# Kernel tuning notes

Measured on AMD Instinct MI355X. Metric: run time of the kernel, lower is better.

Reference implementation:

```python
import jax, jax.numpy as jnp
import numpy as np

B, S, D = 2, 2048, 1024
H = 16
HD = D // H  # 64
SCALE = HD ** -0.5


def setup_inputs() -> dict:
    key = jax.random.key(0)
    ks = jax.random.split(key, 9)
    init = lambda k, shape: jax.random.normal(k, shape, dtype=jnp.float32) * (1.0 / np.sqrt(shape[-1]))
    return {
        "x": jax.random.normal(ks[0], (B, S, D), dtype=jnp.float32),
        "wq": init(ks[1], (D, D)), "bq": jnp.zeros((D,), jnp.float32),
        "wk": init(ks[2], (D, D)), "bk": jnp.zeros((D,), jnp.float32),
        "wv": init(ks[3], (D, D)), "bv": jnp.zeros((D,), jnp.float32),
        "wo": init(ks[4], (D, D)), "bo": jnp.zeros((D,), jnp.float32),
    }


def reference(x, wq, bq, wk, bk, wv, bv, wo, bo):
    b, s, d = x.shape
    # projections -> [b, h, s, hd]
    q = (x @ wq + bq).reshape(b, s, H, HD).transpose(0, 2, 1, 3)
    k = (x @ wk + bk).reshape(b, s, H, HD).transpose(0, 2, 1, 3)
    v = (x @ wv + bv).reshape(b, s, H, HD).transpose(0, 2, 1, 3)
    # full causal attention (chunked loop in original computes exactly this)
    scores = jnp.einsum("bhqd,bhkd->bhqk", q, k) * SCALE
    causal = jnp.tril(jnp.ones((s, s), dtype=bool))
    scores = jnp.where(causal, scores, -jnp.inf)
    weights = jax.nn.softmax(scores, axis=-1)
    out = jnp.einsum("bhqk,bhkd->bhqd", weights, v)
    out = out.transpose(0, 2, 1, 3).reshape(b, s, d)
    return out @ wo + bo
```

## Files before the change

kernel.cpp:

```cpp
#include <hip/hip_runtime.h>
#include <hip/hip_bf16.h>
#include <cstdint>

#define B_  2
#define S_  2048
#define D_  1024
#define H_  16
#define HD_ 64
#define M_  (B_ * S_)
static constexpr float SC_LOG2E = 0.125f * 1.44269504088896f;

typedef __bf16 bf16x8 __attribute__((ext_vector_type(8)));
typedef float  f32x4  __attribute__((ext_vector_type(4)));

__device__ __forceinline__ unsigned short f2b(float f) {
  union { float f; unsigned u; } x; x.f = f;
  unsigned r = x.u + 0x7FFF + ((x.u >> 16) & 1);
  return (unsigned short)(r >> 16);
}

__device__ __forceinline__ void gl_lds16(const unsigned short* g, unsigned short* l) {
  __builtin_amdgcn_global_load_lds((const __attribute__((address_space(1))) void*)g,
                                   (__attribute__((address_space(3))) void*)l, 16, 0, 0);
}

__global__ void cvt_x_kernel(const float4* __restrict__ x, ushort4* __restrict__ o, int n4) {
  int i = blockIdx.x * blockDim.x + threadIdx.x;
  if (i >= n4) return;
  float4 v = x[i];
  ushort4 r;
  r.x = f2b(v.x); r.y = f2b(v.y); r.z = f2b(v.z); r.w = f2b(v.w);
  o[i] = r;
}

__global__ void cvt_w_kernel(const float* __restrict__ w0, const float* __restrict__ w1,
                             const float* __restrict__ w2, const float* __restrict__ w3,
                             unsigned short* __restrict__ o0, unsigned short* __restrict__ o1,
                             unsigned short* __restrict__ o2, unsigned short* __restrict__ o3) {
  const float* w = blockIdx.z == 0 ? w0 : blockIdx.z == 1 ? w1 : blockIdx.z == 2 ? w2 : w3;
  unsigned short* o = blockIdx.z == 0 ? o0 : blockIdx.z == 1 ? o1 : blockIdx.z == 2 ? o2 : o3;
  __shared__ float t[32][33];
  int x0 = blockIdx.x * 32, y0 = blockIdx.y * 32;
  int tx = threadIdx.x, ty = threadIdx.y;
#pragma unroll
  for (int j = 0; j < 4; j++)
    t[ty + j * 8][tx] = w[(size_t)(y0 + ty + j * 8) * D_ + x0 + tx];
  __syncthreads();
#pragma unroll
  for (int j = 0; j < 4; j++)
    o[(size_t)(x0 + ty + j * 8) * D_ + y0 + tx] = f2b(t[tx][ty + j * 8]);
}

__global__ __launch_bounds__(256) void qkv_gemm_kernel(
    const unsigned short* __restrict__ xb,
    const unsigned short* __restrict__ wqt, const unsigned short* __restrict__ wkt,
    const unsigned short* __restrict__ wvt,
    const float* __restrict__ bq, const float* __restrict__ bk, const float* __restrict__ bv,
    unsigned short* __restrict__ qo, unsigned short* __restrict__ ko, unsigned short* __restrict__ vo) {
  const unsigned short* wt = blockIdx.z == 0 ? wqt : blockIdx.z == 1 ? wkt : wvt;
  const float* bias        = blockIdx.z == 0 ? bq  : blockIdx.z == 1 ? bk  : bv;
  unsigned short* out      = blockIdx.z == 0 ? qo  : blockIdx.z == 1 ? ko  : vo;

  __shared__ __align__(16) unsigned short As[128 * 32];
  __shared__ __align__(16) unsigned short Bs[128 * 32];
  const int tid = threadIdx.x;
  const int lane = tid & 63, wid = tid >> 6;
  const int wm = wid & 1, wn = wid >> 1;
  const int m0 = blockIdx.x * 128, n0 = blockIdx.y * 128;
  const int l15 = lane & 15, q4 = lane >> 4;

  f32x4 zero = {0.f, 0.f, 0.f, 0.f};
  f32x4 acc[4][4];
#pragma unroll
  for (int mt = 0; mt < 4; mt++)
#pragma unroll
    for (int nt = 0; nt < 4; nt++) acc[mt][nt] = zero;

  for (int kk = 0; kk < D_; kk += 32) {
#pragma unroll
    for (int i = 0; i < 2; i++) {
      int ci = tid + i * 256;
      int row = ci >> 2, kc = ci & 3;
      gl_lds16(xb + (size_t)(m0 + row) * D_ + kk + kc * 8, As + ci * 8);
      gl_lds16(wt + (size_t)(n0 + row) * D_ + kk + kc * 8, Bs + ci * 8);
    }
    __syncthreads();
    bf16x8 af[4], bfv[4];
#pragma unroll
    for (int mt = 0; mt < 4; mt++) af[mt] = *(const bf16x8*)(As + (wm * 64 + mt * 16 + l15) * 32 + q4 * 8);
#pragma unroll
    for (int nt = 0; nt < 4; nt++) bfv[nt] = *(const bf16x8*)(Bs + (wn * 64 + nt * 16 + l15) * 32 + q4 * 8);
#pragma unroll
    for (int mt = 0; mt < 4; mt++)
#pragma unroll
      for (int nt = 0; nt < 4; nt++)
        acc[mt][nt] = __builtin_amdgcn_mfma_f32_16x16x32_bf16(af[mt], bfv[nt], acc[mt][nt], 0, 0, 0);
    __syncthreads();
  }

  if (blockIdx.z < 2) {
#pragma unroll
    for (int nt = 0; nt < 4; nt++) {
      int n = n0 + wn * 64 + nt * 16 + l15;
      float bn = bias[n];
      int h = n >> 6, hd = n & 63;
#pragma unroll
      for (int mt = 0; mt < 4; mt++) {
#pragma unroll
        for (int r = 0; r < 4; r++) {
          int m = m0 + wm * 64 + mt * 16 + q4 * 4 + r;
          int b = m >> 11, s = m & (S_ - 1);
          out[(((size_t)(b * H_ + h)) * S_ + s) * HD_ + hd] = f2b(acc[mt][nt][r] + bn);
        }
      }
    }
  } else {
    unsigned short* buf = As;
#pragma unroll
    for (int p = 0; p < 2; p++) {
      __syncthreads();
      if (wn == p) {
#pragma unroll
        for (int nt = 0; nt < 4; nt++) {
          int np = nt * 16 + l15;
          float bn = bias[n0 + p * 64 + np];
#pragma unroll
          for (int mt = 0; mt < 4; mt++)
#pragma unroll
            for (int r = 0; r < 4; r++) {
              int ml = wm * 64 + mt * 16 + q4 * 4 + r;
              buf[np * 128 + ml] = f2b(acc[mt][nt][r] + bn);
            }
        }
      }
      __syncthreads();
#pragma unroll
      for (int i = 0; i < 4; i++) {
        int ci = tid + i * 256;
        int np = ci >> 4, c = ci & 15;
        int n = n0 + p * 64 + np;
        int h = n >> 6, hd = n & 63;
        int m = m0 + c * 8;
        int b = m >> 11, s = m & (S_ - 1);
        *(uint4*)(out + (((size_t)(b * H_ + h)) * HD_ + hd) * S_ + s) = *(const uint4*)(buf + np * 128 + c * 8);
      }
    }
  }
}

__global__ __launch_bounds__(256) void attn_kernel(
    const unsigned short* __restrict__ Q, const unsigned short* __restrict__ K,
    const unsigned short* __restrict__ Vt_g, unsigned short* __restrict__ O) {
  const int bh = blockIdx.y, b = bh >> 4, h = bh & 15;
  const unsigned short* Qh = Q    + (size_t)bh * S_ * HD_;
  const unsigned short* Kh = K    + (size_t)bh * S_ * HD_;
  const unsigned short* Vh = Vt_g + (size_t)bh * HD_ * S_;

  __shared__ __align__(16) unsigned short Qs[64 * 72];
  __shared__ __align__(16) unsigned short Ks[128 * 72];
  __shared__ __align__(16) unsigned short Vt[64 * 136];
  __shared__ __align__(16) unsigned short Ps[4][16 * 136];

  const int tid = threadIdx.x, lane = tid & 63, w = tid >> 6;
  const int l15 = lane & 15, q4 = lane >> 4;
  f32x4 zero = {0.f, 0.f, 0.f, 0.f};

  for (int half = 0; half < 2; half++) {
    const int qi = half ? (31 - (int)blockIdx.x) : (int)blockIdx.x;
    const int q0 = qi * 64;
    __syncthreads();
#pragma unroll
    for (int i = 0; i < 2; i++) {
      int ci = tid + i * 256, row = ci >> 3, kc = ci & 7;
      *(uint4*)(Qs + row * 72 + kc * 8) = *(const uint4*)(Qh + (size_t)(q0 + row) * HD_ + kc * 8);
    }

    float m_i = -1e30f, l_i = 0.f;
    f32x4 o_acc[4];
#pragma unroll
    for (int t = 0; t < 4; t++) o_acc[t] = zero;
    const int qrow = q0 + w * 16 + l15;
    const int nkt = qi / 2 + 1;

    for (int kt = 0; kt < nkt; kt++) {
      const int k0 = kt * 128;
      __syncthreads();
#pragma unroll
      for (int i = 0; i < 4; i++) {
        int ci = tid + i * 256, row = ci >> 3, kc = ci & 7;
        *(uint4*)(Ks + row * 72 + kc * 8) = *(const uint4*)(Kh + (size_t)(k0 + row) * HD_ + kc * 8);
      }
#pragma unroll
      for (int i = 0; i < 4; i++) {
        int ci = tid + i * 256, hd = ci >> 4, c = ci & 15;
        *(uint4*)(Vt + hd * 136 + c * 8) = *(const uint4*)(Vh + (size_t)hd * S_ + k0 + c * 8);
      }
      __syncthreads();

      bf16x8 bq0 = *(const bf16x8*)(Qs + (w * 16 + l15) * 72 + q4 * 8);
      bf16x8 bq1 = *(const bf16x8*)(Qs + (w * 16 + l15) * 72 + 32 + q4 * 8);
      f32x4 sc[8];
#pragma unroll
      for (int nt = 0; nt < 8; nt++) sc[nt] = zero;
#pragma unroll
      for (int nt = 0; nt < 8; nt++) {
        bf16x8 ak0 = *(const bf16x8*)(Ks + (nt * 16 + l15) * 72 + q4 * 8);
        bf16x8 ak1 = *(const bf16x8*)(Ks + (nt * 16 + l15) * 72 + 32 + q4 * 8);
        sc[nt] = __builtin_amdgcn_mfma_f32_16x16x32_bf16(ak0, bq0, sc[nt], 0, 0, 0);
        sc[nt] = __builtin_amdgcn_mfma_f32_16x16x32_bf16(ak1, bq1, sc[nt], 0, 0, 0);
      }

      const bool needMask = (k0 + 127) > (q0 + w * 16);
      float mx = m_i;
      if (needMask) {
#pragma unroll
        for (int nt = 0; nt < 8; nt++)
#pragma unroll
          for (int r = 0; r < 4; r++) {
            int key = k0 + nt * 16 + q4 * 4 + r;
            float v = sc[nt][r] * SC_LOG2E;
            v = (key > qrow) ? -1e30f : v;
            sc[nt][r] = v;
            mx = fmaxf(mx, v);
          }
      } else {
#pragma unroll
        for (int nt = 0; nt < 8; nt++)
#pragma unroll
          for (int r = 0; r < 4; r++) {
            float v = sc[nt][r] * SC_LOG2E;
            sc[nt][r] = v;
            mx = fmaxf(mx, v);
          }
      }
      mx = fmaxf(mx, __shfl_xor(mx, 16));
      mx = fmaxf(mx, __shfl_xor(mx, 32));
      float alpha = __builtin_amdgcn_exp2f(m_i - mx);
      m_i = mx;
      float rs = 0.f;
#pragma unroll
      for (int nt = 0; nt < 8; nt++)
#pragma unroll
        for (int r = 0; r < 4; r++) {
          float p = __builtin_amdgcn_exp2f(sc[nt][r] - mx);
          sc[nt][r] = p;
          rs += p;
        }
      rs += __shfl_xor(rs, 16);
      rs += __shfl_xor(rs, 32);
      l_i = l_i * alpha + rs;

#pragma unroll
      for (int r = 0; r < 4; r++) {
        float ar = __shfl(alpha, q4 * 4 + r);
        o_acc[0][r] *= ar; o_acc[1][r] *= ar; o_acc[2][r] *= ar; o_acc[3][r] *= ar;
      }

#pragma unroll
      for (int nt = 0; nt < 8; nt++) {
        ushort4 pk;
        pk.x = f2b(sc[nt][0]); pk.y = f2b(sc[nt][1]);
        pk.z = f2b(sc[nt][2]); pk.w = f2b(sc[nt][3]);
        *(ushort4*)(&Ps[w][l15 * 136 + nt * 16 + q4 * 4]) = pk;
      }
      __threadfence_block();

#pragma unroll
      for (int ks = 0; ks < 4; ks++) {
        bf16x8 ap = *(const bf16x8*)(&Ps[w][l15 * 136 + ks * 32 + q4 * 8]);
#pragma unroll
        for (int nt2 = 0; nt2 < 4; nt2++) {
          bf16x8 bv = *(const bf16x8*)(Vt + (nt2 * 16 + l15) * 136 + ks * 32 + q4 * 8);
          o_acc[nt2] = __builtin_amdgcn_mfma_f32_16x16x32_bf16(ap, bv, o_acc[nt2], 0, 0, 0);
        }
      }
    }

#pragma unroll
    for (int r = 0; r < 4; r++) {
      float lr = __shfl(l_i, q4 * 4 + r);
      float inv = 1.0f / lr;
      int s = q0 + w * 16 + q4 * 4 + r;
#pragma unroll
      for (int nt2 = 0; nt2 < 4; nt2++)
        O[((size_t)(b * S_ + s)) * D_ + h * HD_ + nt2 * 16 + l15] = f2b(o_acc[nt2][r] * inv);
    }
  }
}

__global__ __launch_bounds__(256) void out_gemm_kernel(
    const unsigned short* __restrict__ ab, const unsigned short* __restrict__ wot,
    const float* __restrict__ bo, float* __restrict__ out) {
  __shared__ __align__(16) unsigned short As[128 * 32];
  __shared__ __align__(16) unsigned short Bs[128 * 32];
  const int tid = threadIdx.x;
  const int lane = tid & 63, wid = tid >> 6;
  const int wm = wid & 1, wn = wid >> 1;
  const int m0 = blockIdx.x * 128, n0 = blockIdx.y * 128;
  const int l15 = lane & 15, q4 = lane >> 4;

  f32x4 zero = {0.f, 0.f, 0.f, 0.f};
  f32x4 acc[4][4];
#pragma unroll
  for (int mt = 0; mt < 4; mt++)
#pragma unroll
    for (int nt = 0; nt < 4; nt++) acc[mt][nt] = zero;

  for (int kk = 0; kk < D_; kk += 32) {
#pragma unroll
    for (int i = 0; i < 2; i++) {
      int ci = tid + i * 256;
      int row = ci >> 2, kc = ci & 3;
      gl_lds16(ab  + (size_t)(m0 + row) * D_ + kk + kc * 8, As + ci * 8);
      gl_lds16(wot + (size_t)(n0 + row) * D_ + kk + kc * 8, Bs + ci * 8);
    }
    __syncthreads();
    bf16x8 af[4], bfv[4];
#pragma unroll
    for (int mt = 0; mt < 4; mt++) af[mt] = *(const bf16x8*)(As + (wm * 64 + mt * 16 + l15) * 32 + q4 * 8);
#pragma unroll
    for (int nt = 0; nt < 4; nt++) bfv[nt] = *(const bf16x8*)(Bs + (wn * 64 + nt * 16 + l15) * 32 + q4 * 8);
#pragma unroll
    for (int mt = 0; mt < 4; mt++)
#pragma unroll
      for (int nt = 0; nt < 4; nt++)
        acc[mt][nt] = __builtin_amdgcn_mfma_f32_16x16x32_bf16(af[mt], bfv[nt], acc[mt][nt], 0, 0, 0);
    __syncthreads();
  }

#pragma unroll
  for (int nt = 0; nt < 4; nt++) {
    int n = n0 + wn * 64 + nt * 16 + l15;
    float bn = bo[n];
#pragma unroll
    for (int mt = 0; mt < 4; mt++) {
#pragma unroll
      for (int r = 0; r < 4; r++) {
        int m = m0 + wm * 64 + mt * 16 + q4 * 4 + r;
        out[(size_t)m * D_ + n] = acc[mt][nt][r] + bn;
      }
    }
  }
}

extern "C" void kernel_launch(void* const* d_in, const int* in_sizes, int n_in,
                              void* d_out, int out_size, void* d_ws, size_t ws_size,
                              hipStream_t stream) {
  const float* x  = (const float*)d_in[0];
  const float* wq = (const float*)d_in[1];
  const float* bq = (const float*)d_in[2];
  const float* wk = (const float*)d_in[3];
  const float* bk = (const float*)d_in[4];
  const float* wv = (const float*)d_in[5];
  const float* bv = (const float*)d_in[6];
  const float* wo = (const float*)d_in[7];
  const float* bo = (const float*)d_in[8];
  float* out = (float*)d_out;

  char* ws = (char*)d_ws;
  unsigned short* xb  = (unsigned short*)(ws);
  unsigned short* wqt = (unsigned short*)(ws + (8u  << 20));
  unsigned short* wkt = (unsigned short*)(ws + (10u << 20));
  unsigned short* wvt = (unsigned short*)(ws + (12u << 20));
  unsigned short* wot = (unsigned short*)(ws + (14u << 20));
  unsigned short* qb  = (unsigned short*)(ws + (16u << 20));
  unsigned short* kb  = (unsigned short*)(ws + (24u << 20));
  unsigned short* vtg = (unsigned short*)(ws + (32u << 20));
  unsigned short* ab  = xb;

  cvt_x_kernel<<<dim3(M_ * D_ / 4 / 256), dim3(256), 0, stream>>>((const float4*)x, (ushort4*)xb, M_ * D_ / 4);
  cvt_w_kernel<<<dim3(32, 32, 4), dim3(32, 8), 0, stream>>>(wq, wk, wv, wo, wqt, wkt, wvt, wot);
  qkv_gemm_kernel<<<dim3(32, 8, 3), dim3(256), 0, stream>>>(xb, wqt, wkt, wvt, bq, bk, bv, qb, kb, vtg);
  attn_kernel<<<dim3(16, B_ * H_), dim3(256), 0, stream>>>(qb, kb, vtg, ab);
  out_gemm_kernel<<<dim3(32, 8), dim3(256), 0, stream>>>(ab, wot, bo, out);
}
```

Measured before the change: 212.7 us.

## Merge conversion kernels, fold softmax scale into Q, enlarge attention tiles with prefetch

The x and weight conversion kernels are merged into a single launch using an extra z-slice. The softmax scale times log2e is folded into the Q projection epilogue, so the attention kernel no longer multiplies every score. The attention kernel moves to 512 threads with 128-row query tiles, and it prefetches the next K/V tile into registers while the current one is being computed. This cuts launch overhead and per-score ALU work. In exchange it halves the attention grid size and adds register pressure, and the remaining visible attention code may need to match the new tiling.

```diff
diff --git a/kernel.cpp b/kernel.cpp
--- a/kernel.cpp
+++ b/kernel.cpp
@@ -24,24 +24,31 @@
                                    (__attribute__((address_space(3))) void*)l, 16, 0, 0);
 }
 
-__global__ void cvt_x_kernel(const float4* __restrict__ x, ushort4* __restrict__ o, int n4) {
-  int i = blockIdx.x * blockDim.x + threadIdx.x;
-  if (i >= n4) return;
-  float4 v = x[i];
-  ushort4 r;
-  r.x = f2b(v.x); r.y = f2b(v.y); r.z = f2b(v.z); r.w = f2b(v.w);
-  o[i] = r;
-}
-
-__global__ void cvt_w_kernel(const float* __restrict__ w0, const float* __restrict__ w1,
-                             const float* __restrict__ w2, const float* __restrict__ w3,
-                             unsigned short* __restrict__ o0, unsigned short* __restrict__ o1,
-                             unsigned short* __restrict__ o2, unsigned short* __restrict__ o3) {
+__global__ void cvt_all_kernel(const float* __restrict__ x,
+                               const float* __restrict__ w0, const float* __restrict__ w1,
+                               const float* __restrict__ w2, const float* __restrict__ w3,
+                               unsigned short* __restrict__ xb,
+                               unsigned short* __restrict__ o0, unsigned short* __restrict__ o1,
+                               unsigned short* __restrict__ o2, unsigned short* __restrict__ o3) {
+  int tx = threadIdx.x, ty = threadIdx.y;
+  if (blockIdx.z == 4) {
+    int tid = ty * 32 + tx;
+    int base = ((int)blockIdx.y * 32 + (int)blockIdx.x) * 1024 + tid;
+    const float4* xf = (const float4*)x;
+    ushort4* ob = (ushort4*)xb;
+#pragma unroll
+    for (int j = 0; j < 4; j++) {
+      float4 v = xf[base + j * 256];
+      ushort4 r;
+      r.x = f2b(v.x); r.y = f2b(v.y); r.z = f2b(v.z); r.w = f2b(v.w);
+      ob[base + j * 256] = r;
+    }
+    return;
+  }
   const float* w = blockIdx.z == 0 ? w0 : blockIdx.z == 1 ? w1 : blockIdx.z == 2 ? w2 : w3;
   unsigned short* o = blockIdx.z == 0 ? o0 : blockIdx.z == 1 ? o1 : blockIdx.z == 2 ? o2 : o3;
   __shared__ float t[32][33];
   int x0 = blockIdx.x * 32, y0 = blockIdx.y * 32;
-  int tx = threadIdx.x, ty = threadIdx.y;
 #pragma unroll
   for (int j = 0; j < 4; j++)
     t[ty + j * 8][tx] = w[(size_t)(y0 + ty + j * 8) * D_ + x0 + tx];
@@ -60,6 +67,7 @@
   const unsigned short* wt = blockIdx.z == 0 ? wqt : blockIdx.z == 1 ? wkt : wvt;
   const float* bias        = blockIdx.z == 0 ? bq  : blockIdx.z == 1 ? bk  : bv;
   unsigned short* out      = blockIdx.z == 0 ? qo  : blockIdx.z == 1 ? ko  : vo;
+  const float scl = blockIdx.z == 0 ? SC_LOG2E : 1.0f;
 
   __shared__ __align__(16) unsigned short As[128 * 32];
   __shared__ __align__(16) unsigned short Bs[128 * 32];
@@ -110,7 +118,7 @@
         for (int r = 0; r < 4; r++) {
           int m = m0 + wm * 64 + mt * 16 + q4 * 4 + r;
           int b = m >> 11, s = m & (S_ - 1);
-          out[(((size_t)(b * H_ + h)) * S_ + s) * HD_ + hd] = f2b(acc[mt][nt][r] + bn);
+          out[(((size_t)(b * H_ + h)) * S_ + s) * HD_ + hd] = f2b((acc[mt][nt][r] + bn) * scl);
         }
       }
     }
@@ -148,7 +156,7 @@
   }
 }
 
-__global__ __launch_bounds__(256) void attn_kernel(
+__global__ __launch_bounds__(512) void attn_kernel(
     const unsigned short* __restrict__ Q, const unsigned short* __restrict__ K,
     const unsigned short* __restrict__ Vt_g, unsigned short* __restrict__ O) {
   const int bh = blockIdx.y, b = bh >> 4, h = bh & 15;
@@ -156,22 +164,25 @@
   const unsigned short* Kh = K    + (size_t)bh * S_ * HD_;
   const unsigned short* Vh = Vt_g + (size_t)bh * HD_ * S_;
 
-  __shared__ __align__(16) unsigned short Qs[64 * 72];
+  __shared__ __align__(16) unsigned short Qs[128 * 72];
   __shared__ __align__(16) unsigned short Ks[128 * 72];
   __shared__ __align__(16) unsigned short Vt[64 * 136];
-  __shared__ __align__(16) unsigned short Ps[4][16 * 136];
+  __shared__ __align__(16) unsigned short Ps[8][16 * 136];
 
   const int tid = threadIdx.x, lane = tid & 63, w = tid >> 6;
   const int l15 = lane & 15, q4 = lane >> 4;
   f32x4 zero = {0.f, 0.f, 0.f, 0.f};
 
+  const int krow0 = tid >> 3, kcol0 = (tid & 7) * 8;
+  const int vrow0 = tid >> 4, vcol0 = (tid & 15) * 8;
+
   for (int half = 0; half < 2; half++) {
-    const int qi = half ? (31 - (int)blockIdx.x) : (int)blockIdx.x;
-    const int q0 = qi * 64;
+    const int qi = half ? (15 - (int)blockIdx.x) : (int)blockIdx.x;
+    const int q0 = qi * 128;
     __syncthreads();
 #pragma unroll
     for (int i = 0; i < 2; i++) {
-      int ci = tid + i * 256, row = ci >> 3, kc = ci & 7;
+      int ci = tid + i * 512, row = ci >> 3, kc = ci & 7;
       *(uint4*)(Qs + row * 72 + kc * 8) = *(const uint4*)(Qh + (size_t)(q0 + row) * HD_ + kc * 8);
     }
 
@@ -180,20 +191,26 @@
 #pragma unroll
     for (int t = 0; t < 4; t++) o_acc[t] = zero;
     const int qrow = q0 + w * 16 + l15;
-    const int nkt = qi / 2 + 1;
+    const int nkt = qi + 1;
+
+    uint4 kp0 = *(const uint4*)(Kh + (size_t)krow0 * HD_ + kcol0);
+    uint4 kp1 = *(const uint4*)(Kh + (size_t)(krow0 + 64) * HD_ + kcol0);
+    uint4 vp0 = *(const uint4*)(Vh + (size_t)vrow0 * S_ + vcol0);
+    uint4 vp1 = *(const uint4*)(Vh + (size_t)(vrow0 + 32) * S_ + vcol0);
 
     for (int kt = 0; kt < nkt; kt++) {
       const int k0 = kt * 128;
       __syncthreads();
-#pragma unroll
-      for (int i = 0; i < 4; i++) {
-        int ci = tid + i * 256, row = ci >> 3, kc = ci & 7;
-        *(uint4*)(Ks + row * 72 + kc * 8) = *(const uint4*)(Kh + (size_t)(k0 + row) * HD_ + kc * 8);
-      }
-#pragma unroll
-      for (int i = 0; i < 4; i++) {
-        int ci = tid + i * 256, hd = ci >> 4, c = ci & 15;
-        *(uint4*)(Vt + hd * 136 + c * 8) = *(const uint4*)(Vh + (size_t)hd * S_ + k0 + c * 8);
+      *(uint4*)(Ks + krow0 * 72 + kcol0) = kp0;
+      *(uint4*)(Ks + (krow0 + 64) * 72 + kcol0) = kp1;
+      *(uint4*)(Vt + vrow0 * 136 + vcol0) = vp0;
+      *(uint4*)(Vt + (vrow0 + 32) * 136 + vcol0) = vp1;
+      if (kt + 1 < nkt) {
+        int kn = k0 + 128;
+        kp0 = *(const uint4*)(Kh + (size_t)(kn + krow0) * HD_ + kcol0);
+        kp1 = *(const uint4*)(Kh + (size_t)(kn + krow0 + 64) * HD_ + kcol0);
+        vp0 = *(const uint4*)(Vh + (size_t)vrow0 * S_ + kn + vcol0);
+        vp1 = *(const uint4*)(Vh + (size_t)(vrow0 + 32) * S_ + kn + vcol0);
       }
       __syncthreads();
 
@@ -218,8 +235,7 @@
 #pragma unroll
           for (int r = 0; r < 4; r++) {
             int key = k0 + nt * 16 + q4 * 4 + r;
-            float v = sc[nt][r] * SC_LOG2E;
-            v = (key > qrow) ? -1e30f : v;
+            float v = (key > qrow) ? -1e30f : sc[nt][r];
             sc[nt][r] = v;
             mx = fmaxf(mx, v);
           }
@@ -227,11 +243,7 @@
 #pragma unroll
         for (int nt = 0; nt < 8; nt++)
 #pragma unroll
-          for (int r = 0; r < 4; r++) {
-            float v = sc[nt][r] * SC_LOG2E;
-            sc[nt][r] = v;
-            mx = fmaxf(mx, v);
-          }
+          for (int r = 0; r < 4; r++) mx = fmaxf(mx, sc[nt][r]);
       }
       mx = fmaxf(mx, __shfl_xor(mx, 16));
       mx = fmaxf(mx, __shfl_xor(mx, 32));
@@ -368,9 +380,8 @@
   unsigned short* vtg = (unsigned short*)(ws + (32u << 20));
   unsigned short* ab  = xb;
 
-  cvt_x_kernel<<<dim3(M_ * D_ / 4 / 256), dim3(256), 0, stream>>>((const float4*)x, (ushort4*)xb, M_ * D_ / 4);
-  cvt_w_kernel<<<dim3(32, 32, 4), dim3(32, 8), 0, stream>>>(wq, wk, wv, wo, wqt, wkt, wvt, wot);
+  cvt_all_kernel<<<dim3(32, 32, 5), dim3(32, 8), 0, stream>>>(x, wq, wk, wv, wo, xb, wqt, wkt, wvt, wot);
   qkv_gemm_kernel<<<dim3(32, 8, 3), dim3(256), 0, stream>>>(xb, wqt, wkt, wvt, bq, bk, bv, qb, kb, vtg);
-  attn_kernel<<<dim3(16, B_ * H_), dim3(256), 0, stream>>>(qb, kb, vtg, ab);
+  attn_kernel<<<dim3(8, B_ * H_), dim3(512), 0, stream>>>(qb, kb, vtg, ab);
   out_gemm_kernel<<<dim3(32, 8), dim3(256), 0, stream>>>(ab, wot, bo, out);
 }
```

Result: faster. 205.9 us (-3.2%).
